# Performance work log

Hardware: AMD Instinct MI355X
Metric: run time of the kernel (lower is better)

Reference implementation:

```python
import jax, jax.numpy as jnp
import numpy as np

B, N, D_MODEL, HIDDEN, ACTION_BIN = 4096, 8, 1024, 2048, 256


def setup_inputs() -> dict:
    key = jax.random.key(0)
    k_x, k_w1, k_b1, k_w2, k_b2 = jax.random.split(key, 5)
    # per-action-dim MLP weights stacked along leading n axis
    s1 = 1.0 / np.sqrt(D_MODEL)
    s2 = 1.0 / np.sqrt(HIDDEN)
    return {
        "x": jax.random.normal(k_x, (B, N, D_MODEL), dtype=jnp.float32),
        "W1": jax.random.normal(k_w1, (N, D_MODEL, HIDDEN), dtype=jnp.float32) * s1,
        "b1": jax.random.normal(k_b1, (N, HIDDEN), dtype=jnp.float32) * s1,
        "W2": jax.random.normal(k_w2, (N, HIDDEN, ACTION_BIN), dtype=jnp.float32) * s2,
        "b2": jax.random.normal(k_b2, (N, ACTION_BIN), dtype=jnp.float32) * s2,
    }


def reference(x, W1, b1, W2, b2):
    # Original torch module loops over n slices, each with its own
    # Linear(d_model->hidden) -> ReLU -> Linear(hidden->action_bin).
    # Equivalent grouped/batched matmul over the n axis:
    x = x.astype(jnp.float32)
    h = jnp.einsum('bnd,ndh->bnh', x, W1) + b1[None, :, :]   # [b, n, hidden]
    h = jax.nn.relu(h)
    out = jnp.einsum('bnh,nha->bna', h, W2) + b2[None, :, :]  # [b, n, action_bin]
    return out
```

## Files before the change

### kernel.cpp

```cpp
#include <hip/hip_runtime.h>
#include <stdint.h>

#define BTOT   4096
#define NGRP   8
#define DMODEL 1024
#define HIDDEN 2048
#define ABIN   256

typedef short bf16x8 __attribute__((ext_vector_type(8)));
typedef float f32x4  __attribute__((ext_vector_type(4)));

__device__ __forceinline__ ushort f2bf(float f) {
    union { float f; uint32_t u; } v; v.f = f;
    return (ushort)((v.u + 0x7FFFu + ((v.u >> 16) & 1u)) >> 16);
}

__device__ __forceinline__ void gl_lds16(const ushort* g, ushort* l) {
    __builtin_amdgcn_global_load_lds(
        (const __attribute__((address_space(1))) uint32_t*)g,
        (__attribute__((address_space(3))) uint32_t*)l,
        16, 0, 0);
}

#define W1_TILES ((DMODEL / 32) * (HIDDEN / 32))
#define W2_TILES ((HIDDEN / 32) * (ABIN / 32))
__global__ void transpose_w12(const float* __restrict__ W1, ushort* __restrict__ W1t,
                              const float* __restrict__ W2, ushort* __restrict__ W2t)
{
    __shared__ float tl[32][33];
    const int n = blockIdx.y;
    const float* W; ushort* Wt; int K, N, bx;
    if (blockIdx.x < W1_TILES) {
        W = W1; Wt = W1t; K = DMODEL; N = HIDDEN; bx = blockIdx.x;
    } else {
        W = W2; Wt = W2t; K = HIDDEN; N = ABIN;  bx = blockIdx.x - W1_TILES;
    }
    const int nt = bx % (N / 32);
    const int kt = bx / (N / 32);
    const float* Wn  = W  + (size_t)n * K * N;
    ushort*      Wtn = Wt + (size_t)n * N * K;
    const int tx = threadIdx.x & 31, ty = threadIdx.x >> 5;
#pragma unroll
    for (int j = 0; j < 4; j++)
        tl[ty + 8 * j][tx] = Wn[(size_t)(kt * 32 + ty + 8 * j) * N + nt * 32 + tx];
    __syncthreads();
#pragma unroll
    for (int j = 0; j < 4; j++) {
        const int r = ty + 8 * j;
        Wtn[(size_t)(nt * 32 + r) * K + kt * 32 + tx] = f2bf(tl[tx][r]);
    }
}

__global__ void conv_x(const float* __restrict__ x, ushort* __restrict__ xb,
                       int CH, int cb)
{
    const int flat = blockIdx.x * 256 + threadIdx.x;
    const int d8 = flat & 127;
    const int rem = flat >> 7;
    const int n = rem & 7;
    const int r = rem >> 3;
    const float* src = x + ((size_t)(cb + r) * NGRP + n) * DMODEL + d8 * 8;
    float4 v0 = *(const float4*)(src);
    float4 v1 = *(const float4*)(src + 4);
    bf16x8 p;
    p[0] = (short)f2bf(v0.x); p[1] = (short)f2bf(v0.y);
    p[2] = (short)f2bf(v0.z); p[3] = (short)f2bf(v0.w);
    p[4] = (short)f2bf(v1.x); p[5] = (short)f2bf(v1.y);
    p[6] = (short)f2bf(v1.z); p[7] = (short)f2bf(v1.w);
    *(bf16x8*)(xb + ((size_t)n * CH + r) * DMODEL + d8 * 8) = p;
}

#define REGN(buf,op,half,ks) (sm + ((((buf)*2+(op))*2+(half))*2+(ks))*4096)

template<int MH>
__device__ __forceinline__ void mma_q(f32x4 (&acc)[8][4], const bf16x8 (&af)[4],
                                      const bf16x8 (&bv)[4])
{
#pragma unroll
    for (int m4 = 0; m4 < 4; ++m4)
#pragma unroll
        for (int nf = 0; nf < 4; ++nf)
            acc[MH * 4 + m4][nf] = __builtin_amdgcn_mfma_f32_16x16x32_bf16(
                af[m4], bv[nf], acc[MH * 4 + m4][nf], 0, 0, 0);
}

__global__ __launch_bounds__(512, 2)
void gemm8_1(const ushort* __restrict__ A, const ushort* __restrict__ Bt,
             const float* __restrict__ bias, ushort* __restrict__ h, int CH)
{
    constexpr int K = DMODEL, NDIM = HIDDEN, KT = K / 64;
    const int MT = CH >> 8, NT = NDIM >> 8;
    extern __shared__ ushort sm[];

    const int nwg = gridDim.x;
    const int bid = blockIdx.x;
    const int swz = (bid & 7) * (nwg >> 3) + (bid >> 3);
    const int n   = swz / (MT * NT);
    const int rem = swz - n * (MT * NT);
    const int mt  = rem / NT;
    const int nt  = rem - mt * NT;

    const int tid = threadIdx.x;
    const int l = tid & 63, wid = tid >> 6;
    const int wr = wid >> 2, wc = wid & 3, wc2 = wc >> 1;
    const int lq = l >> 4, lr = l & 15;

    const ushort* Ab = A  + ((size_t)n * CH   + (size_t)mt * 256) * K;
    const ushort* Bb = Bt + ((size_t)n * NDIM + (size_t)nt * 256) * K;

    const int srow = tid >> 2;
    const int sseg = (tid & 3) ^ ((tid >> 3) & 3);

    auto stageA = [&](int b, int T, int ks) {
        const size_t kofs = (size_t)T * 64 + ks * 32 + sseg * 8;
        gl_lds16(Ab + (size_t)srow * K + kofs,         REGN(b, 0, 0, ks) + tid * 8);
        gl_lds16(Ab + (size_t)(128 + srow) * K + kofs, REGN(b, 0, 1, ks) + tid * 8);
    };
    auto stageB = [&](int b, int T, int ks) {
        const size_t kofs = (size_t)T * 64 + ks * 32 + sseg * 8;
        gl_lds16(Bb + (size_t)srow * K + kofs,         REGN(b, 1, 0, ks) + tid * 8);
        gl_lds16(Bb + (size_t)(128 + srow) * K + kofs, REGN(b, 1, 1, ks) + tid * 8);
    };
    auto ldA = [&](bf16x8 (&af)[4], int b, int kk, int mh) {
#pragma unroll
        for (int m4 = 0; m4 < 4; ++m4) {
            const int rh = mh * 64 + m4 * 16 + lr;
            af[m4] = *(const bf16x8*)(REGN(b, 0, wr, kk) + rh * 32 + (lq ^ ((rh >> 1) & 3)) * 8);
        }
    };
    auto ldB = [&](bf16x8 (&bv)[4], int b, int kk) {
#pragma unroll
        for (int nf = 0; nf < 4; ++nf) {
            const int rb = (wc & 1) * 64 + nf * 16 + lr;
            bv[nf] = *(const bf16x8*)(REGN(b, 1, wc2, kk) + rb * 32 + (lq ^ ((rb >> 1) & 3)) * 8);
        }
    };

    f32x4 acc[8][4];
#pragma unroll
    for (int i = 0; i < 8; ++i)
#pragma unroll
        for (int j = 0; j < 4; ++j) acc[i][j] = (f32x4){0.f, 0.f, 0.f, 0.f};

    stageA(0, 0, 0); stageB(0, 0, 0); stageA(0, 0, 1); stageB(0, 0, 1);
    asm volatile("s_waitcnt vmcnt(4)" ::: "memory");
    __builtin_amdgcn_s_barrier();

    bf16x8 aX[4], aY[4], bv0[4], bv1[4];
    ldA(aX, 0, 0, 0); ldB(bv0, 0, 0);

    for (int g = 0; g < KT; ++g) {
        const int c = g & 1;
        const bool ns = (g + 1 < KT);

        ldA(aY, c, 0, 1);
        if (ns) stageA(c ^ 1, g + 1, 0);
        asm volatile("s_waitcnt lgkmcnt(4)" ::: "memory");
        __builtin_amdgcn_sched_barrier(0);
        __builtin_amdgcn_s_setprio(1);
        mma_q<0>(acc, aX, bv0);
        __builtin_amdgcn_s_setprio(0);
        if (ns) asm volatile("s_waitcnt vmcnt(2)" ::: "memory");
        else    asm volatile("s_waitcnt vmcnt(0)" ::: "memory");
        __builtin_amdgcn_s_barrier();

        ldA(aX, c, 1, 0); ldB(bv1, c, 1);
        if (ns) stageB(c ^ 1, g + 1, 0);
        asm volatile("s_waitcnt lgkmcnt(8)" ::: "memory");
        __builtin_amdgcn_sched_barrier(0);
        __builtin_amdgcn_s_setprio(1);
        mma_q<1>(acc, aY, bv0);
        __builtin_amdgcn_s_setprio(0);
        __builtin_amdgcn_s_barrier();

        ldA(aY, c, 1, 1);
        if (ns) stageA(c ^ 1, g + 1, 1);
        asm volatile("s_waitcnt lgkmcnt(4)" ::: "memory");
        __builtin_amdgcn_sched_barrier(0);
        __builtin_amdgcn_s_setprio(1);
        mma_q<0>(acc, aX, bv1);
        __builtin_amdgcn_s_setprio(0);
        __builtin_amdgcn_s_barrier();

        if (ns) stageB(c ^ 1, g + 1, 1);
        asm volatile("s_waitcnt lgkmcnt(0)" ::: "memory");
        __builtin_amdgcn_sched_barrier(0);
        __builtin_amdgcn_s_setprio(1);
        mma_q<1>(acc, aY, bv1);
        __builtin_amdgcn_s_setprio(0);
        if (ns) asm volatile("s_waitcnt vmcnt(4)" ::: "memory");
        __builtin_amdgcn_s_barrier();
        if (ns) { ldA(aX, c ^ 1, 0, 0); ldB(bv0, c ^ 1, 0); }
    }

    __builtin_amdgcn_sched_barrier(0);

    float bias4[4];
#pragma unroll
    for (int nf = 0; nf < 4; ++nf)
        bias4[nf] = bias[(size_t)n * NDIM + nt * 256 + wc * 64 + nf * 16 + lr];
#pragma unroll
    for (int m = 0; m < 8; ++m) {
#pragma unroll
        for (int r = 0; r < 4; ++r) {
            const int row = mt * 256 + wr * 128 + m * 16 + lq * 4 + r;
            ushort* dst = h + ((size_t)n * CH + row) * HIDDEN + nt * 256 + wc * 64 + lr;
#pragma unroll
            for (int nf = 0; nf < 4; ++nf)
                dst[nf * 16] = f2bf(fmaxf(acc[m][nf][r] + bias4[nf], 0.f));
        }
    }
}

__global__ __launch_bounds__(256, 2)
void gemm2w(const ushort* __restrict__ A, const ushort* __restrict__ Bt,
            const float* __restrict__ bias, float* __restrict__ outp,
            int CH, int cb)
{
    constexpr int K = HIDDEN, BK = 64;
    __shared__ __align__(16) ushort As[64 * BK];
    __shared__ __align__(16) ushort Bs[256 * BK];

    const int n  = blockIdx.y;
    const int mt = blockIdx.x;

    const ushort* Ab = A  + ((size_t)n * CH + mt * 64) * K;
    const ushort* Bb = Bt + (size_t)n * ABIN * K;

    const int t = threadIdx.x, l = t & 63, w = t >> 6;
    const int wr = w >> 1, wc = w & 1;
    const int lq = l >> 4, lr = l & 15;

    f32x4 acc[2][8];
#pragma unroll
    for (int i = 0; i < 2; i++)
#pragma unroll
        for (int j = 0; j < 8; j++) acc[i][j] = (f32x4){0.f, 0.f, 0.f, 0.f};

    for (int ki = 0; ki < K / BK; ++ki) {
        const ushort* Ak = Ab + ki * BK;
        const ushort* Bk = Bb + ki * BK;
        __syncthreads();
#pragma unroll
        for (int i = 0; i < 2; i++) {
            const int flat = t + 256 * i;
            const int row = flat >> 3;
            const int seg = (flat & 7) ^ (row & 7);
            gl_lds16(Ak + (size_t)row * K + seg * 8, (ushort*)As + flat * 8);
        }
#pragma unroll
        for (int i = 0; i < 8; i++) {
            const int flat = t + 256 * i;
            const int row = flat >> 3;
            const int seg = (flat & 7) ^ (row & 7);
            gl_lds16(Bk + (size_t)row * K + seg * 8, (ushort*)Bs + flat * 8);
        }
        __syncthreads();

#pragma unroll
        for (int kk = 0; kk < 2; kk++) {
            bf16x8 af[2], bf[8];
#pragma unroll
            for (int m = 0; m < 2; m++) {
                const int row = wr * 32 + m * 16 + lr;
                af[m] = *(const bf16x8*)&As[row * BK + ((kk * 4 + lq) ^ (row & 7)) * 8];
            }
#pragma unroll
            for (int nf = 0; nf < 8; nf++) {
                const int row = wc * 128 + nf * 16 + lr;
                bf[nf] = *(const bf16x8*)&Bs[row * BK + ((kk * 4 + lq) ^ (row & 7)) * 8];
            }
#pragma unroll
            for (int m = 0; m < 2; m++)
#pragma unroll
                for (int nf = 0; nf < 8; nf++)
                    acc[m][nf] = __builtin_amdgcn_mfma_f32_16x16x32_bf16(af[m], bf[nf], acc[m][nf], 0, 0, 0);
        }
    }

    float bias8[8];
#pragma unroll
    for (int nf = 0; nf < 8; nf++)
        bias8[nf] = bias[(size_t)n * ABIN + wc * 128 + nf * 16 + lr];
#pragma unroll
    for (int m = 0; m < 2; m++) {
#pragma unroll
        for (int r = 0; r < 4; r++) {
            const int row = mt * 64 + wr * 32 + m * 16 + lq * 4 + r;
            float* dst = outp + ((size_t)(cb + row) * NGRP + n) * ABIN + wc * 128 + lr;
#pragma unroll
            for (int nf = 0; nf < 8; nf++)
                dst[nf * 16] = acc[m][nf][r] + bias8[nf];
        }
    }
}

extern "C" void kernel_launch(void* const* d_in, const int* in_sizes, int n_in,
                              void* d_out, int out_size, void* d_ws, size_t ws_size,
                              hipStream_t stream)
{
    const float* x  = (const float*)d_in[0];
    const float* W1 = (const float*)d_in[1];
    const float* b1 = (const float*)d_in[2];
    const float* W2 = (const float*)d_in[3];
    const float* b2 = (const float*)d_in[4];

    hipFuncSetAttribute((const void*)gemm8_1,
                        hipFuncAttributeMaxDynamicSharedMemorySize, 131072);

    ushort* W1t = (ushort*)d_ws;
    ushort* W2t = W1t + (size_t)NGRP * HIDDEN * DMODEL;
    ushort* xb  = W2t + (size_t)NGRP * ABIN * HIDDEN;
    const size_t fixed = ((size_t)NGRP * HIDDEN * DMODEL + (size_t)NGRP * ABIN * HIDDEN) * 2;

    int CH = 4096;
    while (CH > 256 && fixed + (size_t)CH * (NGRP * (DMODEL + HIDDEN) * 2) > ws_size) CH >>= 1;
    ushort* h = xb + (size_t)NGRP * CH * DMODEL;

    {
        dim3 g(W1_TILES + W2_TILES, NGRP);
        transpose_w12<<<g, 256, 0, stream>>>(W1, W1t, W2, W2t);
    }

    for (int cb = 0; cb < BTOT; cb += CH) {
        conv_x<<<CH * 4, 256, 0, stream>>>(x, xb, CH, cb);
        const int g1 = NGRP * (CH / 256) * (HIDDEN / 256);
        gemm8_1<<<g1, 512, 131072, stream>>>(xb, W1t, b1, h, CH);
        dim3 g2(CH / 64, NGRP);
        gemm2w<<<g2, 256, 0, stream>>>(h, W2t, b2, (float*)d_out, CH, cb);
    }
}
```

Baseline: 257.7 us.

## Double-buffer gemm2w LDS loads and fuse weight transpose with x conversion

The second GEMM now stages K tiles into two LDS buffers held in dynamic shared memory, so the next tile's global-to-LDS load is issued before the MFMAs on the current tile, which removes one barrier per iteration. The weight transpose and the first chunk's x conversion are merged into a single prep kernel to save one launch and let the two preprocessing jobs share the GPU. Shared memory per block grows to 80 KB, which may reduce occupancy against the requested two blocks per CU.

Measured after the change: 251.5 us. 1.02x faster.

```diff
diff --git a/kernel.cpp b/kernel.cpp
--- a/kernel.cpp
+++ b/kernel.cpp
@@ -24,30 +24,48 @@
 
 #define W1_TILES ((DMODEL / 32) * (HIDDEN / 32))
 #define W2_TILES ((HIDDEN / 32) * (ABIN / 32))
-__global__ void transpose_w12(const float* __restrict__ W1, ushort* __restrict__ W1t,
-                              const float* __restrict__ W2, ushort* __restrict__ W2t)
-{
-    __shared__ float tl[32][33];
-    const int n = blockIdx.y;
-    const float* W; ushort* Wt; int K, N, bx;
-    if (blockIdx.x < W1_TILES) {
-        W = W1; Wt = W1t; K = DMODEL; N = HIDDEN; bx = blockIdx.x;
+#define TP_BLKS  (NGRP * (W1_TILES + W2_TILES))
+__global__ void prep(const float* __restrict__ W1, ushort* __restrict__ W1t,
+                     const float* __restrict__ W2, ushort* __restrict__ W2t,
+                     const float* __restrict__ x, ushort* __restrict__ xb,
+                     int CH, int cb)
+{
+    if (blockIdx.x < TP_BLKS) {
+        __shared__ float tl[32][33];
+        const int n  = blockIdx.x / (W1_TILES + W2_TILES);
+        int bx       = blockIdx.x % (W1_TILES + W2_TILES);
+        const float* W; ushort* Wt; int K, N;
+        if (bx < W1_TILES) { W = W1; Wt = W1t; K = DMODEL; N = HIDDEN; }
+        else               { W = W2; Wt = W2t; K = HIDDEN; N = ABIN; bx -= W1_TILES; }
+        const int nt = bx % (N / 32);
+        const int kt = bx / (N / 32);
+        const float* Wn  = W  + (size_t)n * K * N;
+        ushort*      Wtn = Wt + (size_t)n * N * K;
+        const int tx = threadIdx.x & 31, ty = threadIdx.x >> 5;
+#pragma unroll
+        for (int j = 0; j < 4; j++)
+            tl[ty + 8 * j][tx] = Wn[(size_t)(kt * 32 + ty + 8 * j) * N + nt * 32 + tx];
+        __syncthreads();
+#pragma unroll
+        for (int j = 0; j < 4; j++) {
+            const int r = ty + 8 * j;
+            Wtn[(size_t)(nt * 32 + r) * K + kt * 32 + tx] = f2bf(tl[tx][r]);
+        }
     } else {
-        W = W2; Wt = W2t; K = HIDDEN; N = ABIN;  bx = blockIdx.x - W1_TILES;
-    }
-    const int nt = bx % (N / 32);
-    const int kt = bx / (N / 32);
-    const float* Wn  = W  + (size_t)n * K * N;
-    ushort*      Wtn = Wt + (size_t)n * N * K;
-    const int tx = threadIdx.x & 31, ty = threadIdx.x >> 5;
-#pragma unroll
-    for (int j = 0; j < 4; j++)
-        tl[ty + 8 * j][tx] = Wn[(size_t)(kt * 32 + ty + 8 * j) * N + nt * 32 + tx];
-    __syncthreads();
-#pragma unroll
-    for (int j = 0; j < 4; j++) {
-        const int r = ty + 8 * j;
-        Wtn[(size_t)(nt * 32 + r) * K + kt * 32 + tx] = f2bf(tl[tx][r]);
+        const int flat = (blockIdx.x - TP_BLKS) * 256 + threadIdx.x;
+        const int d8 = flat & 127;
+        const int rem = flat >> 7;
+        const int n = rem & 7;
+        const int r = rem >> 3;
+        const float* src = x + ((size_t)(cb + r) * NGRP + n) * DMODEL + d8 * 8;
+        float4 v0 = *(const float4*)(src);
+        float4 v1 = *(const float4*)(src + 4);
+        bf16x8 p;
+        p[0] = (short)f2bf(v0.x); p[1] = (short)f2bf(v0.y);
+        p[2] = (short)f2bf(v0.z); p[3] = (short)f2bf(v0.w);
+        p[4] = (short)f2bf(v1.x); p[5] = (short)f2bf(v1.y);
+        p[6] = (short)f2bf(v1.z); p[7] = (short)f2bf(v1.w);
+        *(bf16x8*)(xb + ((size_t)n * CH + r) * DMODEL + d8 * 8) = p;
     }
 }
 
@@ -217,9 +235,9 @@
             const float* __restrict__ bias, float* __restrict__ outp,
             int CH, int cb)
 {
-    constexpr int K = HIDDEN, BK = 64;
-    __shared__ __align__(16) ushort As[64 * BK];
-    __shared__ __align__(16) ushort Bs[256 * BK];
+    constexpr int K = HIDDEN, BK = 64, KT = K / BK;
+    constexpr int BUFSZ = (64 + 256) * BK;
+    extern __shared__ ushort sm2[];
 
     const int n  = blockIdx.y;
     const int mt = blockIdx.x;
@@ -231,32 +249,43 @@
     const int wr = w >> 1, wc = w & 1;
     const int lq = l >> 4, lr = l & 15;
 
-    f32x4 acc[2][8];
-#pragma unroll
-    for (int i = 0; i < 2; i++)
-#pragma unroll
-        for (int j = 0; j < 8; j++) acc[i][j] = (f32x4){0.f, 0.f, 0.f, 0.f};
-
-    for (int ki = 0; ki < K / BK; ++ki) {
+    auto stage = [&](int b, int ki) {
+        ushort* As = sm2 + b * BUFSZ;
+        ushort* Bs = As + 64 * BK;
         const ushort* Ak = Ab + ki * BK;
         const ushort* Bk = Bb + ki * BK;
-        __syncthreads();
 #pragma unroll
         for (int i = 0; i < 2; i++) {
             const int flat = t + 256 * i;
             const int row = flat >> 3;
             const int seg = (flat & 7) ^ (row & 7);
-            gl_lds16(Ak + (size_t)row * K + seg * 8, (ushort*)As + flat * 8);
+            gl_lds16(Ak + (size_t)row * K + seg * 8, As + flat * 8);
         }
 #pragma unroll
         for (int i = 0; i < 8; i++) {
             const int flat = t + 256 * i;
             const int row = flat >> 3;
             const int seg = (flat & 7) ^ (row & 7);
-            gl_lds16(Bk + (size_t)row * K + seg * 8, (ushort*)Bs + flat * 8);
-        }
-        __syncthreads();
-
+            gl_lds16(Bk + (size_t)row * K + seg * 8, Bs + flat * 8);
+        }
+    };
+
+    f32x4 acc[2][8];
+#pragma unroll
+    for (int i = 0; i < 2; i++)
+#pragma unroll
+        for (int j = 0; j < 8; j++) acc[i][j] = (f32x4){0.f, 0.f, 0.f, 0.f};
+
+    stage(0, 0);
+    __syncthreads();
+
+    for (int ki = 0; ki < KT; ++ki) {
+        const int c = ki & 1;
+        if (ki + 1 < KT) stage(c ^ 1, ki + 1);
+        __builtin_amdgcn_sched_barrier(0);
+
+        const ushort* As = sm2 + c * BUFSZ;
+        const ushort* Bs = As + 64 * BK;
 #pragma unroll
         for (int kk = 0; kk < 2; kk++) {
             bf16x8 af[2], bf[8];
@@ -276,6 +305,7 @@
                 for (int nf = 0; nf < 8; nf++)
                     acc[m][nf] = __builtin_amdgcn_mfma_f32_16x16x32_bf16(af[m], bf[nf], acc[m][nf], 0, 0, 0);
         }
+        __syncthreads();
     }
 
     float bias8[8];
@@ -307,6 +337,8 @@
 
     hipFuncSetAttribute((const void*)gemm8_1,
                         hipFuncAttributeMaxDynamicSharedMemorySize, 131072);
+    hipFuncSetAttribute((const void*)gemm2w,
+                        hipFuncAttributeMaxDynamicSharedMemorySize, 81920);
 
     ushort* W1t = (ushort*)d_ws;
     ushort* W2t = W1t + (size_t)NGRP * HIDDEN * DMODEL;
@@ -317,16 +349,14 @@
     while (CH > 256 && fixed + (size_t)CH * (NGRP * (DMODEL + HIDDEN) * 2) > ws_size) CH >>= 1;
     ushort* h = xb + (size_t)NGRP * CH * DMODEL;
 
-    {
-        dim3 g(W1_TILES + W2_TILES, NGRP);
-        transpose_w12<<<g, 256, 0, stream>>>(W1, W1t, W2, W2t);
-    }
+    prep<<<TP_BLKS + CH * 4, 256, 0, stream>>>(W1, W1t, W2, W2t, x, xb, CH, 0);
 
     for (int cb = 0; cb < BTOT; cb += CH) {
-        conv_x<<<CH * 4, 256, 0, stream>>>(x, xb, CH, cb);
+        if (cb > 0)
+            conv_x<<<CH * 4, 256, 0, stream>>>(x, xb, CH, cb);
         const int g1 = NGRP * (CH / 256) * (HIDDEN / 256);
         gemm8_1<<<g1, 512, 131072, stream>>>(xb, W1t, b1, h, CH);
         dim3 g2(CH / 64, NGRP);
-        gemm2w<<<g2, 256, 0, stream>>>(h, W2t, b2, (float*)d_out, CH, cb);
-    }
-}
+        gemm2w<<<g2, 256, 81920, stream>>>(h, W2t, b2, (float*)d_out, CH, cb);
+    }
+}
```
